# Performance work log

Hardware: AMD Instinct MI355X
Metric: run time of the kernel (lower is better)

## Reference

```python
import jax, jax.numpy as jnp
import numpy as np

DIM = 512
EDIM = 2 * DIM          # edim(=2) * dim
OUT_DIM = 512
KERNEL_SIZE = 4096
B, L = 4, 4096


def setup_inputs() -> dict:
    key = jax.random.key(0)
    k0, k1, k2, k3, k4 = jax.random.split(key, 5)
    embeddings = jax.random.normal(k0, (B, L, DIM), dtype=jnp.float32)
    logit_alpha = jax.random.uniform(k1, (EDIM,), minval=-3.0, maxval=3.0, dtype=jnp.float32)
    logit_delta = jax.random.uniform(k2, (EDIM,), minval=-3.0, maxval=3.0, dtype=jnp.float32)
    # xavier_uniform: U(-a, a), a = sqrt(6/(fan_in+fan_out))
    a_beta = float(np.sqrt(6.0 / (DIM + EDIM)))
    beta = jax.random.uniform(k3, (DIM, EDIM), minval=-a_beta, maxval=a_beta, dtype=jnp.float32)
    a_eta = float(np.sqrt(6.0 / (EDIM + OUT_DIM)))
    eta = jax.random.uniform(k4, (EDIM, OUT_DIM), minval=-a_eta, maxval=a_eta, dtype=jnp.float32)
    return {"embeddings": embeddings, "logit_alpha": logit_alpha,
            "logit_delta": logit_delta, "beta": beta, "eta": eta}


def reference(embeddings, logit_alpha, logit_delta, beta, eta):
    K = KERNEL_SIZE
    Lseq = embeddings.shape[1]
    # data-dependent EMA decay kernel: kernel[e, t] = p_e * q_e^t
    alpha = jax.nn.sigmoid(logit_alpha)[:, None]            # [E, 1]
    delta = jax.nn.sigmoid(logit_delta)[:, None]            # [E, 1]
    p = alpha
    q = 1.0 - alpha * delta
    len_range = jnp.arange(K, dtype=embeddings.dtype)[None, :]   # [1, K]
    kernel = p * jnp.exp(jnp.log(q) * len_range)            # [E, K]

    u = jnp.einsum('bld,de->ble', embeddings, beta)         # [B, L, E]
    u_T = jnp.swapaxes(u, -1, -2)                           # [B, E, L]

    # forward (causal) direction: flip kernel, full conv via FFT, slice at K-1
    kernel_f = jnp.flip(kernel, axis=-1)
    fft_dim = Lseq + K
    fft_dim = 1 << (fft_dim - 1).bit_length()               # next power of 2 (static)
    inp_fft = jnp.fft.rfft(u_T, n=fft_dim, axis=-1)
    ker_fft = jnp.fft.rfft(kernel_f, n=fft_dim, axis=-1)    # [E, fft_dim//2+1]
    out_full = jnp.fft.irfft(inp_fft * ker_fft, n=fft_dim, axis=-1)
    out_T = out_full[..., K - 1:K - 1 + Lseq].astype(embeddings.dtype)  # [B, E, L]

    out = jnp.swapaxes(out_T, -1, -2)                       # [B, L, E]
    return jnp.einsum('ble,eo->blo', out, eta)              # [B, L, out_dim]
```

## Files before the change

kernel.cpp:

```cpp
#include <hip/hip_runtime.h>
#include <hip/hip_bf16.h>

#define DIM      512
#define EDIM     1024
#define OUTD     512
#define BATCH    4
#define LSEQ     4096
#define MROWS    (BATCH * LSEQ)
#define NCHUNK   64
#define CHUNK    (LSEQ / NCHUNK)

typedef __attribute__((ext_vector_type(8))) __bf16 bf16x8;
typedef __attribute__((ext_vector_type(4))) float  f32x4;

static __device__ __forceinline__ ushort f2b(float f) {
    uint x = __float_as_uint(f);
    x += 0x7fff + ((x >> 16) & 1);
    return (ushort)(x >> 16);
}
static __device__ __forceinline__ float b2f(ushort u) {
    return __uint_as_float(((uint)u) << 16);
}
static __device__ __forceinline__ float sigmoidf(float x) {
    return 1.0f / (1.0f + expf(-x));
}

__global__ void prep_cvt_kernel(const float* __restrict__ emb,
                                ushort* __restrict__ a16,
                                const float* __restrict__ beta,
                                const float* __restrict__ eta,
                                const float* __restrict__ la,
                                const float* __restrict__ ld,
                                ushort* __restrict__ betaT,
                                ushort* __restrict__ etaT,
                                float* __restrict__ p,
                                float* __restrict__ q) {
    int blk = blockIdx.x;
    if (blk < 8192) {
        int i = blk * 256 + threadIdx.x;
        float4 v = ((const float4*)emb)[i];
        ushort4 o;
        o.x = f2b(v.x); o.y = f2b(v.y); o.z = f2b(v.z); o.w = f2b(v.w);
        ((ushort4*)a16)[i] = o;
    } else {
        int i = (blk - 8192) * 256 + threadIdx.x;
        if (i < EDIM * DIM) {
            int n = i / DIM, k = i - n * DIM;
            betaT[i] = f2b(beta[(size_t)k * EDIM + n]);
        }
        if (i < OUTD * EDIM) {
            int o = i / EDIM, e = i - o * EDIM;
            etaT[i] = f2b(eta[(size_t)e * OUTD + o]);
        }
        if (i < EDIM) {
            float a = sigmoidf(la[i]);
            float d = sigmoidf(ld[i]);
            p[i] = a;
            q[i] = 1.0f - a * d;
        }
    }
}

#define MFMA_BF16 __builtin_amdgcn_mfma_f32_16x16x32_bf16
template <int KDIM, int NSHIFT, int OUT_BF16, int DO_AGG>
__global__ __launch_bounds__(512, 2) void gemm256(const ushort* __restrict__ A,
                                                  const ushort* __restrict__ Bt,
                                                  void* __restrict__ Cv,
                                                  const float* __restrict__ qv,
                                                  float* __restrict__ aggp,
                                                  int N) {
    extern __shared__ __align__(16) char smem[];
    const int tid  = threadIdx.x;
    const int lane = tid & 63;
    const int wid  = tid >> 6;
    const int wr   = wid >> 2;
    const int wc   = wid & 3;
    const int l15  = lane & 15;
    const int l4   = lane >> 4;

    const int nwg  = gridDim.x;
    const int flat = ((int)blockIdx.x & 7) * (nwg >> 3) + ((int)blockIdx.x >> 3);
    const int rowBase = (flat >> NSHIFT) << 8;
    const int colBase = (flat & ((1 << NSHIFT) - 1)) << 8;

    const int row0  = tid >> 3;
    const int col16 = (tid & 7) ^ (row0 & 7);
    const ushort* gA0 = A  + (size_t)(rowBase + row0) * KDIM + col16 * 8;
    const ushort* gB0 = Bt + (size_t)(colBase + row0) * KDIM + col16 * 8;
    const int ldsOff = tid * 16;

    const int sw   = (l15 & 7) << 4;
    const int aRow = (wr * 128 + l15) * 128;
    const int bRow = 32768 + (wc * 64 + l15) * 128;
    const int a0 = aRow + ((l4 * 16) ^ sw);
    const int a1 = aRow + ((64 + l4 * 16) ^ sw);
    const int b0 = bRow + ((l4 * 16) ^ sw);
    const int b1 = bRow + ((64 + l4 * 16) ^ sw);

    f32x4 acc[8][4] = {};
    bf16x8 af[4][2], bfr[4][2];

    const int NT = KDIM >> 6;

    auto STAGE = [&](int t) {
        const int boff = (t & 1) << 16;
        const size_t koff = (size_t)t * 64;
        #pragma unroll
        for (int i = 0; i < 4; ++i)
            __builtin_amdgcn_global_load_lds(
                (const __attribute__((address_space(1))) void*)(gA0 + (size_t)i * 64 * KDIM + koff),
                (__attribute__((address_space(3))) void*)(smem + boff + i * 8192 + ldsOff),
                16, 0, 0);
        #pragma unroll
        for (int i = 0; i < 4; ++i)
            __builtin_amdgcn_global_load_lds(
                (const __attribute__((address_space(1))) void*)(gB0 + (size_t)i * 64 * KDIM + koff),
                (__attribute__((address_space(3))) void*)(smem + boff + 32768 + i * 8192 + ldsOff),
                16, 0, 0);
    };

    STAGE(0);
    asm volatile("s_waitcnt vmcnt(0)" ::: "memory");
    __builtin_amdgcn_s_barrier();

    for (int t = 0; t < NT; ++t) {
        const char* sm = smem + ((t & 1) << 16);
        if (t + 1 < NT) STAGE(t + 1);
        #pragma unroll
        for (int m = 0; m < 4; ++m) {
            af[m][0] = *(const bf16x8*)(sm + a0 + m * 2048);
            af[m][1] = *(const bf16x8*)(sm + a1 + m * 2048);
        }
        #pragma unroll
        for (int n = 0; n < 2; ++n) {
            bfr[n][0] = *(const bf16x8*)(sm + b0 + n * 2048);
            bfr[n][1] = *(const bf16x8*)(sm + b1 + n * 2048);
        }
        __builtin_amdgcn_s_barrier();
        __builtin_amdgcn_s_setprio(1);
        #pragma unroll
        for (int m = 0; m < 4; ++m)
            #pragma unroll
            for (int n = 0; n < 2; ++n) {
                acc[m][n] = MFMA_BF16(af[m][0], bfr[n][0], acc[m][n], 0, 0, 0);
                acc[m][n] = MFMA_BF16(af[m][1], bfr[n][1], acc[m][n], 0, 0, 0);
            }
        __builtin_amdgcn_s_setprio(0);
        __builtin_amdgcn_s_barrier();
        #pragma unroll
        for (int n = 2; n < 4; ++n) {
            bfr[n][0] = *(const bf16x8*)(sm + b0 + n * 2048);
            bfr[n][1] = *(const bf16x8*)(sm + b1 + n * 2048);
        }
        __builtin_amdgcn_s_barrier();
        __builtin_amdgcn_s_setprio(1);
        #pragma unroll
        for (int m = 0; m < 4; ++m)
            #pragma unroll
            for (int n = 2; n < 4; ++n) {
                acc[m][n] = MFMA_BF16(af[m][0], bfr[n][0], acc[m][n], 0, 0, 0);
                acc[m][n] = MFMA_BF16(af[m][1], bfr[n][1], acc[m][n], 0, 0, 0);
            }
        __builtin_amdgcn_s_setprio(0);
        __builtin_amdgcn_s_barrier();
        #pragma unroll
        for (int m = 0; m < 4; ++m) {
            af[m][0] = *(const bf16x8*)(sm + a0 + (m + 4) * 2048);
            af[m][1] = *(const bf16x8*)(sm + a1 + (m + 4) * 2048);
        }
        __builtin_amdgcn_s_barrier();
        __builtin_amdgcn_s_setprio(1);
        #pragma unroll
        for (int m = 0; m < 4; ++m)
            #pragma unroll
            for (int n = 0; n < 2; ++n) {
                acc[m + 4][n] = MFMA_BF16(af[m][0], bfr[n][0], acc[m + 4][n], 0, 0, 0);
                acc[m + 4][n] = MFMA_BF16(af[m][1], bfr[n][1], acc[m + 4][n], 0, 0, 0);
            }
        __builtin_amdgcn_s_setprio(0);
        __builtin_amdgcn_s_barrier();
        __builtin_amdgcn_s_setprio(1);
        #pragma unroll
        for (int m = 0; m < 4; ++m)
            #pragma unroll
            for (int n = 2; n < 4; ++n) {
                acc[m + 4][n] = MFMA_BF16(af[m][0], bfr[n][0], acc[m + 4][n], 0, 0, 0);
                acc[m + 4][n] = MFMA_BF16(af[m][1], bfr[n][1], acc[m + 4][n], 0, 0, 0);
            }
        __builtin_amdgcn_s_setprio(0);
        asm volatile("s_waitcnt vmcnt(0)" ::: "memory");
        __builtin_amdgcn_s_barrier();
    }

    #pragma unroll
    for (int m = 0; m < 8; ++m)
        #pragma unroll
        for (int n = 0; n < 4; ++n)
            #pragma unroll
            for (int r = 0; r < 4; ++r) {
                int row = rowBase + wr * 128 + m * 16 + l4 * 4 + r;
                int col = colBase + wc * 64 + n * 16 + l15;
                if (OUT_BF16)
                    ((ushort*)Cv)[(size_t)row * N + col] = f2b(acc[m][n][r]);
                else
                    ((float*)Cv)[(size_t)row * N + col] = acc[m][n][r];
            }

    if (DO_AGG) {
        const int bidx = rowBase >> 12;
        const int chunkBase = ((rowBase & 4095) >> 6) + wr * 2;
        #pragma unroll
        for (int h = 0; h < 2; ++h) {
            #pragma unroll
            for (int n = 0; n < 4; ++n) {
                int col = colBase + wc * 64 + n * 16 + l15;
                float qe = qv[col];
                float q2 = qe * qe, q4 = q2 * q2, q8 = q4 * q4, q16 = q8 * q8;
                float P = 0.0f;
                #pragma unroll
                for (int m = 3; m >= 0; --m) {
                    f32x4 a = acc[h * 4 + m][n];
                    float pm = ((a[3] * qe + a[2]) * qe + a[1]) * qe + a[0];
                    P = P * q16 + pm;
                }
                float ql4 = (l4 & 1 ? q4 : 1.0f) * (l4 & 2 ? q8 : 1.0f);
                P *= ql4;
                P += __shfl_xor(P, 16, 64);
                P += __shfl_xor(P, 32, 64);
                if (l4 == 0)
                    aggp[(((bidx << 6) | (chunkBase + h)) << 10) + col] = P;
            }
        }
    }
}

template <int OUT_BF16>
__global__ __launch_bounds__(256) void gemm_bt(const ushort* __restrict__ A,
                                               const ushort* __restrict__ Bt,
                                               void* __restrict__ Cv,
                                               int M, int N, int K,
                                               int ncolShift) {
    __shared__ ushort smem[16384];
    const int tid  = threadIdx.x;
    const int lane = tid & 63;
    const int wid  = tid >> 6;
    const int wr   = wid >> 1, wc = wid & 1;
    const int l15  = lane & 15;
    const int l4   = lane >> 4;

    const int nwg   = gridDim.x;
    const int chunkw = nwg >> 3;
    const int flat  = (blockIdx.x & 7) * chunkw + (blockIdx.x >> 3);
    const int rowBase = (flat >> ncolShift) << 7;
    const int colBase = (flat & ((1 << ncolShift) - 1)) << 7;

    f32x4 acc[4][4] = {};

    const int nkb = K >> 6;
    for (int kb = 0; kb < nkb; ++kb) {
        #pragma unroll
        for (int r = 0; r < 4; ++r) {
            int c     = r * 256 + tid;
            int row   = c >> 3;
            int col16 = (c & 7) ^ (row & 7);
            const ushort* ga = A  + (size_t)(rowBase + row) * K + kb * 64 + col16 * 8;
            __builtin_amdgcn_global_load_lds(
                (const __attribute__((address_space(1))) void*)ga,
                (__attribute__((address_space(3))) void*)((char*)smem + c * 16),
                16, 0, 0);
            const ushort* gb = Bt + (size_t)(colBase + row) * K + kb * 64 + col16 * 8;
            __builtin_amdgcn_global_load_lds(
                (const __attribute__((address_space(1))) void*)gb,
                (__attribute__((address_space(3))) void*)((char*)smem + 16384 + c * 16),
                16, 0, 0);
        }
        __syncthreads();

        #pragma unroll
        for (int kk = 0; kk < 2; ++kk) {
            bf16x8 af[4], bfr[4];
            #pragma unroll
            for (int m = 0; m < 4; ++m) {
                int row   = wr * 64 + m * 16 + l15;
                int kbyte = kk * 64 + l4 * 16;
                int addr  = row * 128 + (kbyte ^ ((row & 7) << 4));
                af[m] = *(const bf16x8*)((const char*)smem + addr);
            }
            #pragma unroll
            for (int n = 0; n < 4; ++n) {
                int row   = wc * 64 + n * 16 + l15;
                int kbyte = kk * 64 + l4 * 16;
                int addr  = 16384 + row * 128 + (kbyte ^ ((row & 7) << 4));
                bfr[n] = *(const bf16x8*)((const char*)smem + addr);
            }
            #pragma unroll
            for (int m = 0; m < 4; ++m)
                #pragma unroll
                for (int n = 0; n < 4; ++n)
                    acc[m][n] = __builtin_amdgcn_mfma_f32_16x16x32_bf16(
                        af[m], bfr[n], acc[m][n], 0, 0, 0);
        }
        __syncthreads();
    }

    #pragma unroll
    for (int m = 0; m < 4; ++m)
        #pragma unroll
        for (int n = 0; n < 4; ++n)
            #pragma unroll
            for (int r = 0; r < 4; ++r) {
                int row = rowBase + wr * 64 + m * 16 + l4 * 4 + r;
                int col = colBase + wc * 64 + n * 16 + l15;
                if (OUT_BF16)
                    ((ushort*)Cv)[(size_t)row * N + col] = f2b(acc[m][n][r]);
                else
                    ((float*)Cv)[(size_t)row * N + col] = acc[m][n][r];
            }
}

__global__ void scan_apply_kernel(ushort* __restrict__ u,
                                  const float* __restrict__ pv,
                                  const float* __restrict__ qv,
                                  const float* __restrict__ agg) {
    int t = blockIdx.x * blockDim.x + threadIdx.x;
    int e0 = (t & 511) * 2;
    int c  = (t >> 9) & 63;
    int b  = t >> 15;
    float2 qe2 = *(const float2*)(qv + e0);
    float2 pe2 = *(const float2*)(pv + e0);
    float qe[2] = {qe2.x, qe2.y};
    float pe[2] = {pe2.x, pe2.y};
    float qL[2], S[2], w[2];
    #pragma unroll
    for (int k = 0; k < 2; ++k) {
        float x = qe[k];
        #pragma unroll
        for (int s = 0; s < 6; ++s) x *= x;
        qL[k] = x; S[k] = 0.0f; w[k] = 1.0f;
    }
    for (int cp = c + 1; cp < NCHUNK; ++cp) {
        float2 a = *(const float2*)(agg + (((b << 6) | cp) << 10) + e0);
        S[0] += w[0] * a.x;  w[0] *= qL[0];
        S[1] += w[1] * a.y;  w[1] *= qL[1];
    }
    ushort* up = u + ((size_t)(b * LSEQ + c * CHUNK) << 10) + e0;
    #pragma unroll 4
    for (int j = CHUNK - 1; j >= 0; --j) {
        ushort2 uv = *(ushort2*)(up + (size_t)j * EDIM);
        S[0] = b2f(uv.x) + qe[0] * S[0];
        S[1] = b2f(uv.y) + qe[1] * S[1];
        ushort2 ov;
        ov.x = f2b(pe[0] * S[0]);
        ov.y = f2b(pe[1] * S[1]);
        *(ushort2*)(up + (size_t)j * EDIM) = ov;
    }
}

extern "C" void kernel_launch(void* const* d_in, const int* in_sizes, int n_in,
                              void* d_out, int out_size, void* d_ws, size_t ws_size,
                              hipStream_t stream) {
    const float* emb  = (const float*)d_in[0];
    const float* la   = (const float*)d_in[1];
    const float* ld   = (const float*)d_in[2];
    const float* beta = (const float*)d_in[3];
    const float* eta  = (const float*)d_in[4];

    char* ws = (char*)d_ws;
    ushort* a16   = (ushort*)(ws);
    ushort* betaT = (ushort*)(ws + 16777216);
    ushort* etaT  = (ushort*)(ws + 17825792);
    ushort* u     = (ushort*)(ws + 18874368);
    float*  p     = (float*) (ws + 52428800);
    float*  q     = (float*) (ws + 52432896);
    float*  agg   = (float*) (ws + 52436992);

    (void)hipFuncSetAttribute((const void*)gemm256<512, 2, 1, 1>,
                              hipFuncAttributeMaxDynamicSharedMemorySize, 131072);

    prep_cvt_kernel<<<dim3(10240), dim3(256), 0, stream>>>(
        emb, a16, beta, eta, la, ld, betaT, etaT, p, q);

    gemm256<512, 2, 1, 1><<<dim3(256), dim3(512), 131072, stream>>>(
        a16, betaT, (void*)u, q, agg, EDIM);

    scan_apply_kernel<<<dim3(512), dim3(256), 0, stream>>>(u, p, q, agg);

    gemm_bt<0><<<dim3((MROWS / 128) * (OUTD / 128)), dim3(256), 0, stream>>>(
        u, etaT, d_out, MROWS, OUTD, EDIM, 2);
}
```

Measured before the change: 83.74 us.

## Fuse fp32-to-bf16 embedding conversion into the first GEMM's A-tile staging

The separate prep pass that converted the 32 MB fp32 embeddings to a bf16 buffer is removed. The first GEMM now loads fp32 A rows into registers, converts them to bf16 and writes them into swizzled LDS, overlapped with the MFMA work of the current tile. This removes a full read plus write of the activations and one launch's worth of traffic. The beta/eta transposes are also rewritten as LDS-tiled coalesced transposes. In exchange the GEMM reads twice the A bytes from global memory, and the conversion adds register and VALU pressure inside the main loop.

```diff
diff --git a/kernel.cpp b/kernel.cpp
--- a/kernel.cpp
+++ b/kernel.cpp
@@ -25,45 +25,55 @@
     return 1.0f / (1.0f + expf(-x));
 }
 
-__global__ void prep_cvt_kernel(const float* __restrict__ emb,
-                                ushort* __restrict__ a16,
-                                const float* __restrict__ beta,
-                                const float* __restrict__ eta,
-                                const float* __restrict__ la,
-                                const float* __restrict__ ld,
-                                ushort* __restrict__ betaT,
-                                ushort* __restrict__ etaT,
-                                float* __restrict__ p,
-                                float* __restrict__ q) {
+__global__ void prep_kernel(const float* __restrict__ beta,
+                            const float* __restrict__ eta,
+                            const float* __restrict__ la,
+                            const float* __restrict__ ld,
+                            ushort* __restrict__ betaT,
+                            ushort* __restrict__ etaT,
+                            float* __restrict__ p,
+                            float* __restrict__ q) {
+    __shared__ float tf[32][33];
     int blk = blockIdx.x;
-    if (blk < 8192) {
-        int i = blk * 256 + threadIdx.x;
-        float4 v = ((const float4*)emb)[i];
+    if (blk < 512) {
+        int tr = blk >> 5, tc = blk & 31;
+        int r = threadIdx.x >> 3, c4 = (threadIdx.x & 7) * 4;
+        float4 v = *(const float4*)(beta + (size_t)(tr * 32 + r) * EDIM + tc * 32 + c4);
+        tf[r][c4 + 0] = v.x; tf[r][c4 + 1] = v.y;
+        tf[r][c4 + 2] = v.z; tf[r][c4 + 3] = v.w;
+        __syncthreads();
         ushort4 o;
-        o.x = f2b(v.x); o.y = f2b(v.y); o.z = f2b(v.z); o.w = f2b(v.w);
-        ((ushort4*)a16)[i] = o;
+        o.x = f2b(tf[c4 + 0][r]); o.y = f2b(tf[c4 + 1][r]);
+        o.z = f2b(tf[c4 + 2][r]); o.w = f2b(tf[c4 + 3][r]);
+        *(ushort4*)(betaT + (size_t)(tc * 32 + r) * DIM + tr * 32 + c4) = o;
+    } else if (blk < 1024) {
+        int tile = blk - 512;
+        int tr = tile >> 4, tc = tile & 15;
+        int r = threadIdx.x >> 3, c4 = (threadIdx.x & 7) * 4;
+        float4 v = *(const float4*)(eta + (size_t)(tr * 32 + r) * OUTD + tc * 32 + c4);
+        tf[r][c4 + 0] = v.x; tf[r][c4 + 1] = v.y;
+        tf[r][c4 + 2] = v.z; tf[r][c4 + 3] = v.w;
+        __syncthreads();
+        ushort4 o;
+        o.x = f2b(tf[c4 + 0][r]); o.y = f2b(tf[c4 + 1][r]);
+        o.z = f2b(tf[c4 + 2][r]); o.w = f2b(tf[c4 + 3][r]);
+        *(ushort4*)(etaT + (size_t)(tc * 32 + r) * EDIM + tr * 32 + c4) = o;
     } else {
-        int i = (blk - 8192) * 256 + threadIdx.x;
-        if (i < EDIM * DIM) {
-            int n = i / DIM, k = i - n * DIM;
-            betaT[i] = f2b(beta[(size_t)k * EDIM + n]);
-        }
-        if (i < OUTD * EDIM) {
-            int o = i / EDIM, e = i - o * EDIM;
-            etaT[i] = f2b(eta[(size_t)e * OUTD + o]);
-        }
-        if (i < EDIM) {
-            float a = sigmoidf(la[i]);
-            float d = sigmoidf(ld[i]);
-            p[i] = a;
-            q[i] = 1.0f - a * d;
+        #pragma unroll
+        for (int j = 0; j < 4; ++j) {
+            int e = threadIdx.x * 4 + j;
+            float a = sigmoidf(la[e]);
+            float d = sigmoidf(ld[e]);
+            p[e] = a;
+            q[e] = 1.0f - a * d;
         }
     }
 }
 
 #define MFMA_BF16 __builtin_amdgcn_mfma_f32_16x16x32_bf16
-template <int KDIM, int NSHIFT, int OUT_BF16, int DO_AGG>
-__global__ __launch_bounds__(512, 2) void gemm256(const ushort* __restrict__ A,
+template <int KDIM, int NSHIFT, int A_FP32, int OUT_BF16, int DO_AGG>
+__global__ __launch_bounds__(512, 2) void gemm256(const ushort* __restrict__ Ab,
+                                                  const float* __restrict__ Af,
                                                   const ushort* __restrict__ Bt,
                                                   void* __restrict__ Cv,
                                                   const float* __restrict__ qv,
@@ -85,9 +95,12 @@
 
     const int row0  = tid >> 3;
     const int col16 = (tid & 7) ^ (row0 & 7);
-    const ushort* gA0 = A  + (size_t)(rowBase + row0) * KDIM + col16 * 8;
+    const ushort* gA0 = Ab + (size_t)(rowBase + row0) * KDIM + col16 * 8;
     const ushort* gB0 = Bt + (size_t)(colBase + row0) * KDIM + col16 * 8;
     const int ldsOff = tid * 16;
+    const int ar = tid >> 1;
+    const int ah = tid & 1;
+    const float* gAf = Af + (size_t)(rowBase + ar) * KDIM + ah * 32;
 
     const int sw   = (l15 & 7) << 4;
     const int aRow = (wr * 128 + l15) * 128;
@@ -99,18 +112,25 @@
 
     f32x4 acc[8][4] = {};
     bf16x8 af[4][2], bfr[4][2];
+    float4 aReg[8];
 
     const int NT = KDIM >> 6;
 
-    auto STAGE = [&](int t) {
+    auto ISSUE = [&](int t) {
         const int boff = (t & 1) << 16;
-        const size_t koff = (size_t)t * 64;
-        #pragma unroll
-        for (int i = 0; i < 4; ++i)
-            __builtin_amdgcn_global_load_lds(
-                (const __attribute__((address_space(1))) void*)(gA0 + (size_t)i * 64 * KDIM + koff),
-                (__attribute__((address_space(3))) void*)(smem + boff + i * 8192 + ldsOff),
-                16, 0, 0);
+        const int koff = t * 64;
+        if (A_FP32) {
+            const float4* src = (const float4*)(gAf + koff);
+            #pragma unroll
+            for (int i = 0; i < 8; ++i) aReg[i] = src[i];
+        } else {
+            #pragma unroll
+            for (int i = 0; i < 4; ++i)
+                __builtin_amdgcn_global_load_lds(
+                    (const __attribute__((address_space(1))) void*)(gA0 + (size_t)i * 64 * KDIM + koff),
+                    (__attribute__((address_space(3))) void*)(smem + boff + i * 8192 + ldsOff),
+                    16, 0, 0);
+        }
         #pragma unroll
         for (int i = 0; i < 4; ++i)
             __builtin_amdgcn_global_load_lds(
@@ -119,13 +139,33 @@
                 16, 0, 0);
     };
 
-    STAGE(0);
-    asm volatile("s_waitcnt vmcnt(0)" ::: "memory");
+    auto STAGE_WRITE = [&](int t) {
+        const int boff = (t & 1) << 16;
+        const int swr  = (ar & 7) << 4;
+        char* base = smem + boff + ar * 128;
+        #pragma unroll
+        for (int i = 0; i < 4; ++i) {
+            uint4 v;
+            v.x = (uint)f2b(aReg[2 * i].x)     | ((uint)f2b(aReg[2 * i].y) << 16);
+            v.y = (uint)f2b(aReg[2 * i].z)     | ((uint)f2b(aReg[2 * i].w) << 16);
+            v.z = (uint)f2b(aReg[2 * i + 1].x) | ((uint)f2b(aReg[2 * i + 1].y) << 16);
+            v.w = (uint)f2b(aReg[2 * i + 1].z) | ((uint)f2b(aReg[2 * i + 1].w) << 16);
+            int slot = ah * 4 + i;
+            *(uint4*)(base + ((slot * 16) ^ swr)) = v;
+        }
+    };
+
+    ISSUE(0);
+    if (A_FP32) {
+        asm volatile("s_waitcnt vmcnt(4)" ::: "memory");
+        STAGE_WRITE(0);
+    }
+    asm volatile("s_waitcnt vmcnt(0) lgkmcnt(0)" ::: "memory");
     __builtin_amdgcn_s_barrier();
 
     for (int t = 0; t < NT; ++t) {
         const char* sm = smem + ((t & 1) << 16);
-        if (t + 1 < NT) STAGE(t + 1);
+        if (t + 1 < NT) ISSUE(t + 1);
         #pragma unroll
         for (int m = 0; m < 4; ++m) {
             af[m][0] = *(const bf16x8*)(sm + a0 + m * 2048);
@@ -163,6 +203,10 @@
             }
         __builtin_amdgcn_s_setprio(0);
         __builtin_amdgcn_s_barrier();
+        if (A_FP32 && t + 1 < NT) {
+            asm volatile("s_waitcnt vmcnt(4)" ::: "memory");
+            STAGE_WRITE(t + 1);
+        }
         #pragma unroll
         for (int m = 0; m < 4; ++m) {
             af[m][0] = *(const bf16x8*)(sm + a0 + (m + 4) * 2048);
@@ -188,7 +232,7 @@
                 acc[m + 4][n] = MFMA_BF16(af[m][1], bfr[n][1], acc[m + 4][n], 0, 0, 0);
             }
         __builtin_amdgcn_s_setprio(0);
-        asm volatile("s_waitcnt vmcnt(0)" ::: "memory");
+        asm volatile("s_waitcnt vmcnt(0) lgkmcnt(0)" ::: "memory");
         __builtin_amdgcn_s_barrier();
     }
 
@@ -366,22 +410,21 @@
     const float* eta  = (const float*)d_in[4];
 
     char* ws = (char*)d_ws;
-    ushort* a16   = (ushort*)(ws);
-    ushort* betaT = (ushort*)(ws + 16777216);
-    ushort* etaT  = (ushort*)(ws + 17825792);
-    ushort* u     = (ushort*)(ws + 18874368);
-    float*  p     = (float*) (ws + 52428800);
-    float*  q     = (float*) (ws + 52432896);
-    float*  agg   = (float*) (ws + 52436992);
-
-    (void)hipFuncSetAttribute((const void*)gemm256<512, 2, 1, 1>,
+    ushort* betaT = (ushort*)(ws);
+    ushort* etaT  = (ushort*)(ws + 1048576);
+    ushort* u     = (ushort*)(ws + 2097152);
+    float*  p     = (float*) (ws + 35651584);
+    float*  q     = (float*) (ws + 35655680);
+    float*  agg   = (float*) (ws + 35659776);
+
+    (void)hipFuncSetAttribute((const void*)gemm256<512, 2, 1, 1, 1>,
                               hipFuncAttributeMaxDynamicSharedMemorySize, 131072);
 
-    prep_cvt_kernel<<<dim3(10240), dim3(256), 0, stream>>>(
-        emb, a16, beta, eta, la, ld, betaT, etaT, p, q);
-
-    gemm256<512, 2, 1, 1><<<dim3(256), dim3(512), 131072, stream>>>(
-        a16, betaT, (void*)u, q, agg, EDIM);
+    prep_kernel<<<dim3(1025), dim3(256), 0, stream>>>(beta, eta, la, ld,
+                                                      betaT, etaT, p, q);
+
+    gemm256<512, 2, 1, 1, 1><<<dim3(256), dim3(512), 131072, stream>>>(
+        nullptr, emb, betaT, (void*)u, q, agg, EDIM);
 
     scan_apply_kernel<<<dim3(512), dim3(256), 0, stream>>>(u, p, q, agg);
 
```

After: 95.02 us. +13.5%, slower.
